# Kernel tuning notes

Hardware: AMD Instinct MI355X
Metric: run time of the kernel (lower is better)

Reference implementation:

```python
import jax, jax.numpy as jnp
import numpy as np

B, S, D, H = 4, 2048, 1024, 16
DH = D // H

def setup_inputs() -> dict:
    key = jax.random.key(0)
    ks = jax.random.split(key, 4)
    scale = 1.0 / np.sqrt(D)
    x = jax.random.normal(ks[0], (B, S, D), dtype=jnp.float32)
    Wq = jax.random.normal(ks[1], (D, D), dtype=jnp.float32) * scale
    Wk = jax.random.normal(ks[2], (D, D), dtype=jnp.float32) * scale
    Wv = jax.random.normal(ks[3], (D, D), dtype=jnp.float32) * scale
    bq = jnp.zeros((D,), dtype=jnp.float32)
    bk = jnp.zeros((D,), dtype=jnp.float32)
    bv = jnp.zeros((D,), dtype=jnp.float32)
    # causal mask, broadcastable to [B, H, S, S]; mask==0 positions get -inf
    mask = jnp.tril(jnp.ones((S, S), dtype=bool))[None, None, :, :]
    return {"x": x, "mask": mask, "Wq": Wq, "bq": bq, "Wk": Wk, "bk": bk, "Wv": Wv, "bv": bv}

def reference(x, mask, Wq, bq, Wk, bk, Wv, bv):
    b, s, d = x.shape
    def proj(W, bias):
        # nn.Linear: x @ W.T + b, then split heads -> [b, H, s, DH]
        y = jnp.einsum('bsd,ed->bse', x, W) + bias
        return y.reshape(b, s, H, DH).transpose(0, 2, 1, 3)
    q = proj(Wq, bq)
    k = proj(Wk, bk)
    v = proj(Wv, bv)
    scores = jnp.einsum('bhqd,bhkd->bhqk', q, k) / jnp.sqrt(jnp.float32(DH))
    scores = jnp.where(mask, scores, -jnp.inf)
    attn = jax.nn.softmax(scores, axis=-1)
    out = jnp.einsum('bhqk,bhkd->bhqd', attn, v)
    return out.transpose(0, 2, 1, 3).reshape(b, s, d)
```

## Files before the change

kernel.cpp:

```cpp
#include <hip/hip_runtime.h>
#include <hip/hip_bf16.h>
#include <stdint.h>

typedef unsigned short u16;
typedef unsigned int   u32;
typedef short bf16x8 __attribute__((ext_vector_type(8)));
typedef float f32x4  __attribute__((ext_vector_type(4)));

typedef bf16x8 __attribute__((__may_alias__)) bf16x8_a;
typedef uint4  __attribute__((__may_alias__)) uint4_a;
typedef uint2  __attribute__((__may_alias__)) uint2_a;
typedef float4 __attribute__((__may_alias__)) float4_a;

#define MFMA_BF16(a,b,c) __builtin_amdgcn_mfma_f32_16x16x32_bf16((a),(b),(c),0,0,0)
#define L2E 1.44269504088896340736f

#define SEQ 2048
#define DMODEL 1024
#define NH 16
#define DH 64

__device__ __forceinline__ u32 pack_bf2(float a, float b) {
  union { __hip_bfloat162 h; u32 u; } c;
  c.h = __float22bfloat162_rn(make_float2(a, b));
  return c.u;
}

__device__ __forceinline__ u16 f2bf(float f) {
  u32 u = __builtin_bit_cast(u32, f);
  u += 0x7FFFu + ((u >> 16) & 1u);
  return (u16)(u >> 16);
}

__device__ __forceinline__ void gl_lds16(const u16* g, u16* l) {
  __builtin_amdgcn_global_load_lds(
      (const __attribute__((address_space(1))) void*)g,
      (__attribute__((address_space(3))) void*)l, 16, 0, 0);
}

__global__ __launch_bounds__(256) void cvt_x_bf16(
    const float* __restrict__ s, u16* __restrict__ d, int n8)
{
  int i = blockIdx.x * 256 + threadIdx.x;
  const int stride = gridDim.x * 256;
  for (; i < n8; i += stride) {
    const float4_a* p = (const float4_a*)(s + (size_t)i * 8);
    float4 a = p[0], b = p[1];
    uint4 o;
    o.x = pack_bf2(a.x, a.y); o.y = pack_bf2(a.z, a.w);
    o.z = pack_bf2(b.x, b.y); o.w = pack_bf2(b.z, b.w);
    *(uint4_a*)(d + (size_t)i * 8) = o;
  }
}

__global__ __launch_bounds__(256) void cvt_w_bf16(
    const float* __restrict__ wq, const float* __restrict__ wk, const float* __restrict__ wv,
    u16* __restrict__ oq, u16* __restrict__ ok, u16* __restrict__ ov)
{
  const float* s = (blockIdx.y == 0) ? wq : (blockIdx.y == 1) ? wk : wv;
  u16*         d = (blockIdx.y == 0) ? oq : (blockIdx.y == 1) ? ok : ov;
  const int i = blockIdx.x * 256 + threadIdx.x;
  const float4_a* p = (const float4_a*)(s + (size_t)i * 8);
  float4 a = p[0], b = p[1];
  uint4 o;
  o.x = pack_bf2(a.x, a.y); o.y = pack_bf2(a.z, a.w);
  o.z = pack_bf2(b.x, b.y); o.w = pack_bf2(b.z, b.w);
  *(uint4_a*)(d + (size_t)i * 8) = o;
}

__global__ __launch_bounds__(256, 4) void qkv_gemm_bf(
    const u16* __restrict__ Xb,
    const u16* __restrict__ Wqb, const u16* __restrict__ Wkb, const u16* __restrict__ Wvb,
    const float* __restrict__ Bq, const float* __restrict__ Bk, const float* __restrict__ Bv,
    u16* __restrict__ Qo, u16* __restrict__ Ko, u16* __restrict__ Vo)
{
  __shared__ u16 As[2][128 * 32];
  __shared__ u16 Bs[2][128 * 32];

  const int tid  = threadIdx.x;
  const int lane = tid & 63;
  const int wid  = tid >> 6;
  const int l16  = lane & 15;
  const int quad = lane >> 4;
  const int wm   = (wid >> 1) * 64;
  const int wn   = (wid & 1) * 64;

  const int m0 = blockIdx.x * 128;
  const int n0 = blockIdx.y * 128;
  const int pj = blockIdx.z;

  const u16*   Wb   = (pj == 0) ? Wqb : (pj == 1) ? Wkb : Wvb;
  const float* Bias = (pj == 0) ? Bq : (pj == 1) ? Bk : Bv;
  u16*         Out  = (pj == 0) ? Qo : (pj == 1) ? Ko : Vo;
  const float scale = (pj == 0) ? 0.125f : 1.0f;

  f32x4 acc[4][4];
#pragma unroll
  for (int i = 0; i < 4; i++)
#pragma unroll
    for (int j = 0; j < 4; j++) acc[i][j] = (f32x4){0.f, 0.f, 0.f, 0.f};

  const int lr = lane >> 2;
  const int lc = (lane & 3) * 8;

  const u16* Arow = Xb + (size_t)m0 * DMODEL;
  const u16* Brow = Wb + (size_t)n0 * DMODEL;

  const int NT = DMODEL / 32;

#pragma unroll
  for (int c = 0; c < 2; c++) {
    const int band = c * 64 + wid * 16;
    gl_lds16(Arow + (size_t)(band + lr) * DMODEL + 0 + lc, &As[0][band * 32]);
    gl_lds16(Brow + (size_t)(band + lr) * DMODEL + 0 + lc, &Bs[0][band * 32]);
  }
#pragma unroll
  for (int c = 0; c < 2; c++) {
    const int band = c * 64 + wid * 16;
    gl_lds16(Arow + (size_t)(band + lr) * DMODEL + 32 + lc, &As[1][band * 32]);
    gl_lds16(Brow + (size_t)(band + lr) * DMODEL + 32 + lc, &Bs[1][band * 32]);
  }

  for (int t = 0; t < NT; ++t) {
    const int cur = t & 1;
    if (t < NT - 1) asm volatile("s_waitcnt vmcnt(4)" ::: "memory");
    else            asm volatile("s_waitcnt vmcnt(0)" ::: "memory");
    __builtin_amdgcn_s_barrier();

    bf16x8 a[4], b[4];
#pragma unroll
    for (int mt = 0; mt < 4; mt++)
      a[mt] = *(const bf16x8_a*)&As[cur][(wm + mt * 16 + l16) * 32 + quad * 8];
#pragma unroll
    for (int nt = 0; nt < 4; nt++)
      b[nt] = *(const bf16x8_a*)&Bs[cur][(wn + nt * 16 + l16) * 32 + quad * 8];

    asm volatile("s_waitcnt lgkmcnt(0)" ::: "memory");
    __builtin_amdgcn_sched_barrier(0);
    __builtin_amdgcn_s_barrier();

    if (t + 2 < NT) {
      const int kt2 = (t + 2) * 32;
#pragma unroll
      for (int c = 0; c < 2; c++) {
        const int band = c * 64 + wid * 16;
        gl_lds16(Arow + (size_t)(band + lr) * DMODEL + kt2 + lc, &As[cur][band * 32]);
        gl_lds16(Brow + (size_t)(band + lr) * DMODEL + kt2 + lc, &Bs[cur][band * 32]);
      }
    }

#pragma unroll
    for (int mt = 0; mt < 4; mt++)
#pragma unroll
      for (int nt = 0; nt < 4; nt++)
        acc[mt][nt] = MFMA_BF16(a[mt], b[nt], acc[mt][nt]);
  }

  if (pj == 2) {
#pragma unroll
    for (int mt = 0; mt < 4; mt++) {
#pragma unroll
      for (int nt = 0; nt < 4; nt++) {
        const int n = n0 + wn + nt * 16 + l16;
        const float bias = Bias[n];
        const int h = n >> 6, dh = n & 63;
        const int m = m0 + wm + mt * 16 + quad * 4;
        const int bb = m >> 11, ss = m & 2047;
        uint2 pk;
        pk.x = pack_bf2(acc[mt][nt][0] + bias, acc[mt][nt][1] + bias);
        pk.y = pack_bf2(acc[mt][nt][2] + bias, acc[mt][nt][3] + bias);
        *(uint2_a*)&Out[((size_t)(bb * NH + h) * DH + dh) * SEQ + ss] = pk;
      }
    }
  } else {
#pragma unroll
    for (int mt = 0; mt < 4; mt++) {
#pragma unroll
      for (int nt = 0; nt < 4; nt++) {
        const int n = n0 + wn + nt * 16 + l16;
        const float bias = Bias[n];
        const int h = n >> 6, dh = n & 63;
#pragma unroll
        for (int r = 0; r < 4; r++) {
          const int m = m0 + wm + mt * 16 + quad * 4 + r;
          const int bb = m >> 11, ss = m & 2047;
          Out[((((size_t)bb * NH + h) * SEQ + ss) << 6) + dh] = f2bf((acc[mt][nt][r] + bias) * scale);
        }
      }
    }
  }
}

__global__ __launch_bounds__(256, 2) void qkv_gemm(
    const float* __restrict__ X,
    const float* __restrict__ Wq, const float* __restrict__ Wk, const float* __restrict__ Wv,
    const float* __restrict__ Bq, const float* __restrict__ Bk, const float* __restrict__ Bv,
    u16* __restrict__ Qo, u16* __restrict__ Ko, u16* __restrict__ Vo)
{
  __shared__ u16 As[128 * 32];
  __shared__ u16 Bs[128 * 32];

  const int tid  = threadIdx.x;
  const int lane = tid & 63;
  const int wid  = tid >> 6;
  const int l16  = lane & 15;
  const int quad = lane >> 4;
  const int wm   = (wid >> 1) * 64;
  const int wn   = (wid & 1) * 64;

  const int m0 = blockIdx.x * 128;
  const int n0 = blockIdx.y * 128;
  const int pj = blockIdx.z;

  const float* W    = (pj == 0) ? Wq : (pj == 1) ? Wk : Wv;
  const float* Bias = (pj == 0) ? Bq : (pj == 1) ? Bk : Bv;
  u16*         Out  = (pj == 0) ? Qo : (pj == 1) ? Ko : Vo;
  const float scale = (pj == 0) ? 0.125f : 1.0f;

  f32x4 acc[4][4];
#pragma unroll
  for (int i = 0; i < 4; i++)
#pragma unroll
    for (int j = 0; j < 4; j++) acc[i][j] = (f32x4){0.f, 0.f, 0.f, 0.f};

  float4 gX[4], gW[4];
#pragma unroll
  for (int i = 0; i < 4; i++) {
    const int ch = i * 256 + tid;
    const int r = ch >> 3, c = ch & 7;
    gX[i] = *(const float4_a*)(X + (size_t)(m0 + r) * DMODEL + c * 4);
    gW[i] = *(const float4_a*)(W + (size_t)(n0 + r) * DMODEL + c * 4);
  }

  for (int kt = 0; kt < DMODEL; kt += 32) {
    __syncthreads();
#pragma unroll
    for (int i = 0; i < 4; i++) {
      const int ch = i * 256 + tid;
      const int r = ch >> 3, c = ch & 7;
      uint2 xp, wp;
      xp.x = pack_bf2(gX[i].x, gX[i].y);  xp.y = pack_bf2(gX[i].z, gX[i].w);
      wp.x = pack_bf2(gW[i].x, gW[i].y);  wp.y = pack_bf2(gW[i].z, gW[i].w);
      *(uint2_a*)&As[r * 32 + c * 4] = xp;
      *(uint2_a*)&Bs[r * 32 + c * 4] = wp;
    }
    __syncthreads();

    if (kt + 32 < DMODEL) {
#pragma unroll
      for (int i = 0; i < 4; i++) {
        const int ch = i * 256 + tid;
        const int r = ch >> 3, c = ch & 7;
        gX[i] = *(const float4_a*)(X + (size_t)(m0 + r) * DMODEL + kt + 32 + c * 4);
        gW[i] = *(const float4_a*)(W + (size_t)(n0 + r) * DMODEL + kt + 32 + c * 4);
      }
    }

    bf16x8 a[4], b[4];
#pragma unroll
    for (int mt = 0; mt < 4; mt++)
      a[mt] = *(const bf16x8_a*)&As[(wm + mt * 16 + l16) * 32 + quad * 8];
#pragma unroll
    for (int nt = 0; nt < 4; nt++)
      b[nt] = *(const bf16x8_a*)&Bs[(wn + nt * 16 + l16) * 32 + quad * 8];
#pragma unroll
    for (int mt = 0; mt < 4; mt++)
#pragma unroll
      for (int nt = 0; nt < 4; nt++)
        acc[mt][nt] = MFMA_BF16(a[mt], b[nt], acc[mt][nt]);
  }

  if (pj == 2) {
#pragma unroll
    for (int mt = 0; mt < 4; mt++) {
#pragma unroll
      for (int nt = 0; nt < 4; nt++) {
        const int n = n0 + wn + nt * 16 + l16;
        const float bias = Bias[n];
        const int h = n >> 6, dh = n & 63;
        const int m = m0 + wm + mt * 16 + quad * 4;
        const int bb = m >> 11, ss = m & 2047;
        uint2 pk;
        pk.x = pack_bf2(acc[mt][nt][0] + bias, acc[mt][nt][1] + bias);
        pk.y = pack_bf2(acc[mt][nt][2] + bias, acc[mt][nt][3] + bias);
        *(uint2_a*)&Out[((size_t)(bb * NH + h) * DH + dh) * SEQ + ss] = pk;
      }
    }
  } else {
#pragma unroll
    for (int mt = 0; mt < 4; mt++) {
#pragma unroll
      for (int nt = 0; nt < 4; nt++) {
        const int n = n0 + wn + nt * 16 + l16;
        const float bias = Bias[n];
        const int h = n >> 6, dh = n & 63;
#pragma unroll
        for (int r = 0; r < 4; r++) {
          const int m = m0 + wm + mt * 16 + quad * 4 + r;
          const int bb = m >> 11, ss = m & 2047;
          Out[((((size_t)bb * NH + h) * SEQ + ss) << 6) + dh] = f2bf((acc[mt][nt][r] + bias) * scale);
        }
      }
    }
  }
}

__global__ __launch_bounds__(256, 4) void flash_attn(
    const u16* __restrict__ Q, const u16* __restrict__ K, const u16* __restrict__ VT,
    float* __restrict__ O)
{
  __shared__ u16 Ks[64 * 72];
  __shared__ u16 VTs[64 * 72];
  __shared__ u16 Ps[4 * 32 * 72];

  const int tid  = threadIdx.x;
  const int lane = tid & 63;
  const int wid  = tid >> 6;
  const int l16  = lane & 15;
  const int quad = lane >> 4;

  const int idx = blockIdx.x;
  const int y = idx >> 6, g = y >> 2, r4 = y & 3;
  const int qt = (g & 1) ? ((g == 1 ? 0 : 4) + r4) : ((g == 0 ? 15 : 11) - r4);
  const int bh  = idx & 63;
  const int bb = bh >> 4, hh = bh & 15;
  const int qbase = qt * 128;

  const u16* Qh = Q  + (size_t)bh * (SEQ * DH);
  const u16* Kh = K  + (size_t)bh * (SEQ * DH);
  const u16* Vh = VT + (size_t)bh * (DH * SEQ);

#pragma unroll
  for (int i = 0; i < 4; i++) {
    const int ch = i * 256 + tid;
    const int r = ch >> 3, c = ch & 7;
    *(uint4_a*)&Ps[r * 72 + c * 8] = *(const uint4_a*)(Qh + (size_t)(qbase + r) * DH + c * 8);
  }
  __syncthreads();

  u16* Pw = &Ps[wid * 32 * 72];
  bf16x8 qf[2][2];
#pragma unroll
  for (int ct = 0; ct < 2; ct++)
#pragma unroll
    for (int ks = 0; ks < 2; ks++)
      qf[ct][ks] = *(const bf16x8_a*)&Pw[(ct * 16 + l16) * 72 + ks * 32 + quad * 8];

  f32x4 o[4][2];
#pragma unroll
  for (int dt = 0; dt < 4; dt++)
#pragma unroll
    for (int ct = 0; ct < 2; ct++) o[dt][ct] = (f32x4){0.f, 0.f, 0.f, 0.f};

  float mold[2] = {-1e30f, -1e30f};
  float lsum[2] = {0.f, 0.f};

  const int jmax = 2 * qt + 1;

  uint4 gK[2], gV[2];
#pragma unroll
  for (int i = 0; i < 2; i++) {
    const int ch = i * 256 + tid;
    gK[i] = *(const uint4_a*)(Kh + (size_t)(ch >> 3) * DH + (ch & 7) * 8);
    gV[i] = *(const uint4_a*)(Vh + (size_t)(ch >> 3) * SEQ + (ch & 7) * 8);
  }

  for (int j = 0; j <= jmax; j++) {
    __syncthreads();
#pragma unroll
    for (int i = 0; i < 2; i++) {
      const int ch = i * 256 + tid;
      *(uint4_a*)&Ks[(ch >> 3) * 72 + (ch & 7) * 8]  = gK[i];
      *(uint4_a*)&VTs[(ch >> 3) * 72 + (ch & 7) * 8] = gV[i];
    }
    __syncthreads();

    if (j < jmax) {
      const int kb2 = (j + 1) * 64;
#pragma unroll
      for (int i = 0; i < 2; i++) {
        const int ch = i * 256 + tid;
        gK[i] = *(const uint4_a*)(Kh + (size_t)(kb2 + (ch >> 3)) * DH + (ch & 7) * 8);
        gV[i] = *(const uint4_a*)(Vh + (size_t)(ch >> 3) * SEQ + kb2 + (ch & 7) * 8);
      }
    }

    f32x4 s[4][2];
#pragma unroll
    for (int rt = 0; rt < 4; rt++) {
      bf16x8 ka0 = *(const bf16x8_a*)&Ks[(rt * 16 + l16) * 72 + 0 + quad * 8];
      bf16x8 ka1 = *(const bf16x8_a*)&Ks[(rt * 16 + l16) * 72 + 32 + quad * 8];
#pragma unroll
      for (int ct = 0; ct < 2; ct++) {
        f32x4 c = (f32x4){0.f, 0.f, 0.f, 0.f};
        c = MFMA_BF16(ka0, qf[ct][0], c);
        c = MFMA_BF16(ka1, qf[ct][1], c);
        s[rt][ct] = c;
      }
    }

    if (j >= (qt << 1)) {
      const int kvb = j * 64;
#pragma unroll
      for (int rt = 0; rt < 4; rt++)
#pragma unroll
        for (int ct = 0; ct < 2; ct++) {
          const int ql = qbase + wid * 32 + ct * 16 + l16;
#pragma unroll
          for (int r = 0; r < 4; r++) {
            const int kvg = kvb + rt * 16 + quad * 4 + r;
            if (kvg > ql) s[rt][ct][r] = -1e30f;
          }
        }
    }

#pragma unroll
    for (int ct = 0; ct < 2; ct++) {
      float m0_ = fmaxf(fmaxf(s[0][ct][0], s[0][ct][1]), fmaxf(s[0][ct][2], s[0][ct][3]));
      float m1_ = fmaxf(fmaxf(s[1][ct][0], s[1][ct][1]), fmaxf(s[1][ct][2], s[1][ct][3]));
      float m2_ = fmaxf(fmaxf(s[2][ct][0], s[2][ct][1]), fmaxf(s[2][ct][2], s[2][ct][3]));
      float m3_ = fmaxf(fmaxf(s[3][ct][0], s[3][ct][1]), fmaxf(s[3][ct][2], s[3][ct][3]));
      float mt = fmaxf(fmaxf(m0_, m1_), fmaxf(m2_, m3_));
      mt = fmaxf(mt, __shfl_xor(mt, 16));
      mt = fmaxf(mt, __shfl_xor(mt, 32));

      if (!__all(mt - mold[ct] <= 8.0f)) {
        const float mnew = fmaxf(mold[ct], mt);
        const float a = __builtin_amdgcn_exp2f((mold[ct] - mnew) * L2E);
        lsum[ct] *= a;
        mold[ct] = mnew;
#pragma unroll
        for (int dt = 0; dt < 4; dt++)
#pragma unroll
          for (int r = 0; r < 4; r++) o[dt][ct][r] *= a;
      }
      const float mref = mold[ct];

#pragma unroll
      for (int rt = 0; rt < 4; rt++)
#pragma unroll
        for (int r = 0; r < 4; r++)
          s[rt][ct][r] = __builtin_amdgcn_exp2f((s[rt][ct][r] - mref) * L2E);

      float t0 = (s[0][ct][0] + s[0][ct][1]) + (s[0][ct][2] + s[0][ct][3]);
      float t1 = (s[1][ct][0] + s[1][ct][1]) + (s[1][ct][2] + s[1][ct][3]);
      float t2 = (s[2][ct][0] + s[2][ct][1]) + (s[2][ct][2] + s[2][ct][3]);
      float t3 = (s[3][ct][0] + s[3][ct][1]) + (s[3][ct][2] + s[3][ct][3]);
      float ls = (t0 + t1) + (t2 + t3);
      ls += __shfl_xor(ls, 16);
      ls += __shfl_xor(ls, 32);
      lsum[ct] += ls;
    }

#pragma unroll
    for (int rt = 0; rt < 4; rt++) {
#pragma unroll
      for (int ct = 0; ct < 2; ct++) {
        uint2 pk;
        pk.x = pack_bf2(s[rt][ct][0], s[rt][ct][1]);
        pk.y = pack_bf2(s[rt][ct][2], s[rt][ct][3]);
        *(uint2_a*)&Pw[(ct * 16 + l16) * 72 + rt * 16 + quad * 4] = pk;
      }
    }
    asm volatile("s_waitcnt lgkmcnt(0)" ::: "memory");

#pragma unroll
    for (int ks2 = 0; ks2 < 2; ks2++) {
      bf16x8 vt[4], pb[2];
#pragma unroll
      for (int dt = 0; dt < 4; dt++)
        vt[dt] = *(const bf16x8_a*)&VTs[(dt * 16 + l16) * 72 + ks2 * 32 + quad * 8];
#pragma unroll
      for (int ct = 0; ct < 2; ct++)
        pb[ct] = *(const bf16x8_a*)&Pw[(ct * 16 + l16) * 72 + ks2 * 32 + quad * 8];
#pragma unroll
      for (int dt = 0; dt < 4; dt++)
#pragma unroll
        for (int ct = 0; ct < 2; ct++)
          o[dt][ct] = MFMA_BF16(vt[dt], pb[ct], o[dt][ct]);
    }
  }

#pragma unroll
  for (int ct = 0; ct < 2; ct++) {
    const float inv = 1.0f / lsum[ct];
    const int qg = qbase + wid * 32 + ct * 16 + l16;
    float* orow = O + (size_t)((size_t)bb * SEQ + qg) * DMODEL + hh * 64;
#pragma unroll
    for (int dt = 0; dt < 4; dt++) {
      float4 v4;
      v4.x = o[dt][ct][0] * inv;  v4.y = o[dt][ct][1] * inv;
      v4.z = o[dt][ct][2] * inv;  v4.w = o[dt][ct][3] * inv;
      *(float4_a*)&orow[dt * 16 + quad * 4] = v4;
    }
  }
}

__global__ void paintf(float* out, int n, float v) {
  int i = blockIdx.x * 256 + threadIdx.x;
  if (i < n) out[i] = v;
}

extern "C" void kernel_launch(void* const* d_in, const int* in_sizes, int n_in,
                              void* d_out, int out_size, void* d_ws, size_t ws_size,
                              hipStream_t stream) {
  float* out = (float*)d_out;

  const size_t elems  = (size_t)4 * SEQ * DMODEL;
  const size_t welems = (size_t)DMODEL * DMODEL;
  const size_t need_old = 3 * elems * sizeof(u16);
  const size_t need_new = (4 * elems + 3 * welems) * sizeof(u16);

  if (ws_size < need_old) {
    paintf<<<(out_size + 255) / 256, 256, 0, stream>>>(out, out_size, 3.0e38f);
    return;
  }

  const float* x  = (const float*)d_in[0];
  const float* Wq = (const float*)d_in[2];
  const float* bq = (const float*)d_in[3];
  const float* Wk = (const float*)d_in[4];
  const float* bk = (const float*)d_in[5];
  const float* Wv = (const float*)d_in[6];
  const float* bv = (const float*)d_in[7];

  u16* q = (u16*)d_ws;
  u16* k = q + elems;
  u16* v = k + elems;

  if (ws_size >= need_new) {
    u16* xb  = v + elems;
    u16* wqb = xb + elems;
    u16* wkb = wqb + welems;
    u16* wvb = wkb + welems;
    cvt_x_bf16<<<2048, 256, 0, stream>>>(x, xb, (int)(elems / 8));
    cvt_w_bf16<<<dim3(512, 3), 256, 0, stream>>>(Wq, Wk, Wv, wqb, wkb, wvb);
    qkv_gemm_bf<<<dim3(64, 8, 3), 256, 0, stream>>>(xb, wqb, wkb, wvb, bq, bk, bv, q, k, v);
  } else {
    qkv_gemm<<<dim3(64, 8, 3), 256, 0, stream>>>(x, Wq, Wk, Wv, bq, bk, bv, q, k, v);
  }

  flash_attn<<<1024, 256, 0, stream>>>(q, k, v, out);
}
```

Baseline: 287.5 us.

## Loop GEMM blocks over two N tiles, MFMA row sums, simpler attention tile order

The bf16 QKV GEMM now has each block compute two 128-wide N subtiles in sequence, which halves the grid in y and lowers the occupancy hint from 4 to 3. In flash attention, the per-row softmax sum is now accumulated by an MFMA against a vector of ones instead of adds and cross-lane shuffles, and the max shuffle runs only when a rescale is needed. The interleaved query-tile ordering is replaced by a plain descending order. These changes aim to cut shuffle and ALU overhead and reduce launch count, but risk worse load balance across the causal tiles and less latency hiding in the GEMM.

```diff
diff --git a/kernel.cpp b/kernel.cpp
--- a/kernel.cpp
+++ b/kernel.cpp
@@ -68,7 +68,7 @@
   *(uint4_a*)(d + (size_t)i * 8) = o;
 }
 
-__global__ __launch_bounds__(256, 4) void qkv_gemm_bf(
+__global__ __launch_bounds__(256, 3) void qkv_gemm_bf(
     const u16* __restrict__ Xb,
     const u16* __restrict__ Wqb, const u16* __restrict__ Wkb, const u16* __restrict__ Wvb,
     const float* __restrict__ Bq, const float* __restrict__ Bk, const float* __restrict__ Bv,
@@ -86,7 +86,6 @@
   const int wn   = (wid & 1) * 64;
 
   const int m0 = blockIdx.x * 128;
-  const int n0 = blockIdx.y * 128;
   const int pj = blockIdx.z;
 
   const u16*   Wb   = (pj == 0) ? Wqb : (pj == 1) ? Wkb : Wvb;
@@ -94,61 +93,182 @@
   u16*         Out  = (pj == 0) ? Qo : (pj == 1) ? Ko : Vo;
   const float scale = (pj == 0) ? 0.125f : 1.0f;
 
-  f32x4 acc[4][4];
-#pragma unroll
-  for (int i = 0; i < 4; i++)
-#pragma unroll
-    for (int j = 0; j < 4; j++) acc[i][j] = (f32x4){0.f, 0.f, 0.f, 0.f};
-
   const int lr = lane >> 2;
   const int lc = (lane & 3) * 8;
 
   const u16* Arow = Xb + (size_t)m0 * DMODEL;
-  const u16* Brow = Wb + (size_t)n0 * DMODEL;
-
   const int NT = DMODEL / 32;
 
-#pragma unroll
-  for (int c = 0; c < 2; c++) {
-    const int band = c * 64 + wid * 16;
-    gl_lds16(Arow + (size_t)(band + lr) * DMODEL + 0 + lc, &As[0][band * 32]);
-    gl_lds16(Brow + (size_t)(band + lr) * DMODEL + 0 + lc, &Bs[0][band * 32]);
-  }
-#pragma unroll
-  for (int c = 0; c < 2; c++) {
-    const int band = c * 64 + wid * 16;
-    gl_lds16(Arow + (size_t)(band + lr) * DMODEL + 32 + lc, &As[1][band * 32]);
-    gl_lds16(Brow + (size_t)(band + lr) * DMODEL + 32 + lc, &Bs[1][band * 32]);
-  }
-
-  for (int t = 0; t < NT; ++t) {
-    const int cur = t & 1;
-    if (t < NT - 1) asm volatile("s_waitcnt vmcnt(4)" ::: "memory");
-    else            asm volatile("s_waitcnt vmcnt(0)" ::: "memory");
-    __builtin_amdgcn_s_barrier();
+  for (int nsub = 0; nsub < 2; ++nsub) {
+    const int n0 = blockIdx.y * 256 + nsub * 128;
+    const u16* Brow = Wb + (size_t)n0 * DMODEL;
+
+    f32x4 acc[4][4];
+#pragma unroll
+    for (int i = 0; i < 4; i++)
+#pragma unroll
+      for (int j = 0; j < 4; j++) acc[i][j] = (f32x4){0.f, 0.f, 0.f, 0.f};
+
+#pragma unroll
+    for (int c = 0; c < 2; c++) {
+      const int band = c * 64 + wid * 16;
+      gl_lds16(Arow + (size_t)(band + lr) * DMODEL + 0 + lc, &As[0][band * 32]);
+      gl_lds16(Brow + (size_t)(band + lr) * DMODEL + 0 + lc, &Bs[0][band * 32]);
+    }
+#pragma unroll
+    for (int c = 0; c < 2; c++) {
+      const int band = c * 64 + wid * 16;
+      gl_lds16(Arow + (size_t)(band + lr) * DMODEL + 32 + lc, &As[1][band * 32]);
+      gl_lds16(Brow + (size_t)(band + lr) * DMODEL + 32 + lc, &Bs[1][band * 32]);
+    }
+
+    for (int t = 0; t < NT; ++t) {
+      const int cur = t & 1;
+      if (t < NT - 1) asm volatile("s_waitcnt vmcnt(4)" ::: "memory");
+      else            asm volatile("s_waitcnt vmcnt(0)" ::: "memory");
+      __builtin_amdgcn_s_barrier();
+
+      bf16x8 a[4], b[4];
+#pragma unroll
+      for (int mt = 0; mt < 4; mt++)
+        a[mt] = *(const bf16x8_a*)&As[cur][(wm + mt * 16 + l16) * 32 + quad * 8];
+#pragma unroll
+      for (int nt = 0; nt < 4; nt++)
+        b[nt] = *(const bf16x8_a*)&Bs[cur][(wn + nt * 16 + l16) * 32 + quad * 8];
+
+      asm volatile("s_waitcnt lgkmcnt(0)" ::: "memory");
+      __builtin_amdgcn_sched_barrier(0);
+      __builtin_amdgcn_s_barrier();
+
+      if (t + 2 < NT) {
+        const int kt2 = (t + 2) * 32;
+#pragma unroll
+        for (int c = 0; c < 2; c++) {
+          const int band = c * 64 + wid * 16;
+          gl_lds16(Arow + (size_t)(band + lr) * DMODEL + kt2 + lc, &As[cur][band * 32]);
+          gl_lds16(Brow + (size_t)(band + lr) * DMODEL + kt2 + lc, &Bs[cur][band * 32]);
+        }
+      }
+
+#pragma unroll
+      for (int mt = 0; mt < 4; mt++)
+#pragma unroll
+        for (int nt = 0; nt < 4; nt++)
+          acc[mt][nt] = MFMA_BF16(a[mt], b[nt], acc[mt][nt]);
+    }
+
+    if (pj == 2) {
+#pragma unroll
+      for (int mt = 0; mt < 4; mt++) {
+#pragma unroll
+        for (int nt = 0; nt < 4; nt++) {
+          const int n = n0 + wn + nt * 16 + l16;
+          const float bias = Bias[n];
+          const int h = n >> 6, dh = n & 63;
+          const int m = m0 + wm + mt * 16 + quad * 4;
+          const int bb = m >> 11, ss = m & 2047;
+          uint2 pk;
+          pk.x = pack_bf2(acc[mt][nt][0] + bias, acc[mt][nt][1] + bias);
+          pk.y = pack_bf2(acc[mt][nt][2] + bias, acc[mt][nt][3] + bias);
+          *(uint2_a*)&Out[((size_t)(bb * NH + h) * DH + dh) * SEQ + ss] = pk;
+        }
+      }
+    } else {
+#pragma unroll
+      for (int mt = 0; mt < 4; mt++) {
+#pragma unroll
+        for (int nt = 0; nt < 4; nt++) {
+          const int n = n0 + wn + nt * 16 + l16;
+          const float bias = Bias[n];
+          const int h = n >> 6, dh = n & 63;
+#pragma unroll
+          for (int r = 0; r < 4; r++) {
+            const int m = m0 + wm + mt * 16 + quad * 4 + r;
+            const int bb = m >> 11, ss = m & 2047;
+            Out[((((size_t)bb * NH + h) * SEQ + ss) << 6) + dh] = f2bf((acc[mt][nt][r] + bias) * scale);
+          }
+        }
+      }
+    }
+
+    if (nsub == 0) {
+      asm volatile("s_waitcnt vmcnt(0)" ::: "memory");
+    }
+  }
+}
+
+__global__ __launch_bounds__(256, 2) void qkv_gemm(
+    const float* __restrict__ X,
+    const float* __restrict__ Wq, const float* __restrict__ Wk, const float* __restrict__ Wv,
+    const float* __restrict__ Bq, const float* __restrict__ Bk, const float* __restrict__ Bv,
+    u16* __restrict__ Qo, u16* __restrict__ Ko, u16* __restrict__ Vo)
+{
+  __shared__ u16 As[128 * 32];
+  __shared__ u16 Bs[128 * 32];
+
+  const int tid  = threadIdx.x;
+  const int lane = tid & 63;
+  const int wid  = tid >> 6;
+  const int l16  = lane & 15;
+  const int quad = lane >> 4;
+  const int wm   = (wid >> 1) * 64;
+  const int wn   = (wid & 1) * 64;
+
+  const int m0 = blockIdx.x * 128;
+  const int n0 = blockIdx.y * 128;
+  const int pj = blockIdx.z;
+
+  const float* W    = (pj == 0) ? Wq : (pj == 1) ? Wk : Wv;
+  const float* Bias = (pj == 0) ? Bq : (pj == 1) ? Bk : Bv;
+  u16*         Out  = (pj == 0) ? Qo : (pj == 1) ? Ko : Vo;
+  const float scale = (pj == 0) ? 0.125f : 1.0f;
+
+  f32x4 acc[4][4];
+#pragma unroll
+  for (int i = 0; i < 4; i++)
+#pragma unroll
+    for (int j = 0; j < 4; j++) acc[i][j] = (f32x4){0.f, 0.f, 0.f, 0.f};
+
+  float4 gX[4], gW[4];
+#pragma unroll
+  for (int i = 0; i < 4; i++) {
+    const int ch = i * 256 + tid;
+    const int r = ch >> 3, c = ch & 7;
+    gX[i] = *(const float4_a*)(X + (size_t)(m0 + r) * DMODEL + c * 4);
+    gW[i] = *(const float4_a*)(W + (size_t)(n0 + r) * DMODEL + c * 4);
+  }
+
+  for (int kt = 0; kt < DMODEL; kt += 32) {
+    __syncthreads();
+#pragma unroll
+    for (int i = 0; i < 4; i++) {
+      const int ch = i * 256 + tid;
+      const int r = ch >> 3, c = ch & 7;
+      uint2 xp, wp;
+      xp.x = pack_bf2(gX[i].x, gX[i].y);  xp.y = pack_bf2(gX[i].z, gX[i].w);
+      wp.x = pack_bf2(gW[i].x, gW[i].y);  wp.y = pack_bf2(gW[i].z, gW[i].w);
+      *(uint2_a*)&As[r * 32 + c * 4] = xp;
+      *(uint2_a*)&Bs[r * 32 + c * 4] = wp;
+    }
+    __syncthreads();
+
+    if (kt + 32 < DMODEL) {
+#pragma unroll
+      for (int i = 0; i < 4; i++) {
+        const int ch = i * 256 + tid;
+        const int r = ch >> 3, c = ch & 7;
+        gX[i] = *(const float4_a*)(X + (size_t)(m0 + r) * DMODEL + kt + 32 + c * 4);
+        gW[i] = *(const float4_a*)(W + (size_t)(n0 + r) * DMODEL + kt + 32 + c * 4);
+      }
+    }
 
     bf16x8 a[4], b[4];
 #pragma unroll
     for (int mt = 0; mt < 4; mt++)
-      a[mt] = *(const bf16x8_a*)&As[cur][(wm + mt * 16 + l16) * 32 + quad * 8];
+      a[mt] = *(const bf16x8_a*)&As[(wm + mt * 16 + l16) * 32 + quad * 8];
 #pragma unroll
     for (int nt = 0; nt < 4; nt++)
-      b[nt] = *(const bf16x8_a*)&Bs[cur][(wn + nt * 16 + l16) * 32 + quad * 8];
-
-    asm volatile("s_waitcnt lgkmcnt(0)" ::: "memory");
-    __builtin_amdgcn_sched_barrier(0);
-    __builtin_amdgcn_s_barrier();
-
-    if (t + 2 < NT) {
-      const int kt2 = (t + 2) * 32;
-#pragma unroll
-      for (int c = 0; c < 2; c++) {
-        const int band = c * 64 + wid * 16;
-        gl_lds16(Arow + (size_t)(band + lr) * DMODEL + kt2 + lc, &As[cur][band * 32]);
-        gl_lds16(Brow + (size_t)(band + lr) * DMODEL + kt2 + lc, &Bs[cur][band * 32]);
-      }
-    }
-
+      b[nt] = *(const bf16x8_a*)&Bs[(wn + nt * 16 + l16) * 32 + quad * 8];
 #pragma unroll
     for (int mt = 0; mt < 4; mt++)
 #pragma unroll
@@ -191,120 +311,6 @@
   }
 }
 
-__global__ __launch_bounds__(256, 2) void qkv_gemm(
-    const float* __restrict__ X,
-    const float* __restrict__ Wq, const float* __restrict__ Wk, const float* __restrict__ Wv,
-    const float* __restrict__ Bq, const float* __restrict__ Bk, const float* __restrict__ Bv,
-    u16* __restrict__ Qo, u16* __restrict__ Ko, u16* __restrict__ Vo)
-{
-  __shared__ u16 As[128 * 32];
-  __shared__ u16 Bs[128 * 32];
-
-  const int tid  = threadIdx.x;
-  const int lane = tid & 63;
-  const int wid  = tid >> 6;
-  const int l16  = lane & 15;
-  const int quad = lane >> 4;
-  const int wm   = (wid >> 1) * 64;
-  const int wn   = (wid & 1) * 64;
-
-  const int m0 = blockIdx.x * 128;
-  const int n0 = blockIdx.y * 128;
-  const int pj = blockIdx.z;
-
-  const float* W    = (pj == 0) ? Wq : (pj == 1) ? Wk : Wv;
-  const float* Bias = (pj == 0) ? Bq : (pj == 1) ? Bk : Bv;
-  u16*         Out  = (pj == 0) ? Qo : (pj == 1) ? Ko : Vo;
-  const float scale = (pj == 0) ? 0.125f : 1.0f;
-
-  f32x4 acc[4][4];
-#pragma unroll
-  for (int i = 0; i < 4; i++)
-#pragma unroll
-    for (int j = 0; j < 4; j++) acc[i][j] = (f32x4){0.f, 0.f, 0.f, 0.f};
-
-  float4 gX[4], gW[4];
-#pragma unroll
-  for (int i = 0; i < 4; i++) {
-    const int ch = i * 256 + tid;
-    const int r = ch >> 3, c = ch & 7;
-    gX[i] = *(const float4_a*)(X + (size_t)(m0 + r) * DMODEL + c * 4);
-    gW[i] = *(const float4_a*)(W + (size_t)(n0 + r) * DMODEL + c * 4);
-  }
-
-  for (int kt = 0; kt < DMODEL; kt += 32) {
-    __syncthreads();
-#pragma unroll
-    for (int i = 0; i < 4; i++) {
-      const int ch = i * 256 + tid;
-      const int r = ch >> 3, c = ch & 7;
-      uint2 xp, wp;
-      xp.x = pack_bf2(gX[i].x, gX[i].y);  xp.y = pack_bf2(gX[i].z, gX[i].w);
-      wp.x = pack_bf2(gW[i].x, gW[i].y);  wp.y = pack_bf2(gW[i].z, gW[i].w);
-      *(uint2_a*)&As[r * 32 + c * 4] = xp;
-      *(uint2_a*)&Bs[r * 32 + c * 4] = wp;
-    }
-    __syncthreads();
-
-    if (kt + 32 < DMODEL) {
-#pragma unroll
-      for (int i = 0; i < 4; i++) {
-        const int ch = i * 256 + tid;
-        const int r = ch >> 3, c = ch & 7;
-        gX[i] = *(const float4_a*)(X + (size_t)(m0 + r) * DMODEL + kt + 32 + c * 4);
-        gW[i] = *(const float4_a*)(W + (size_t)(n0 + r) * DMODEL + kt + 32 + c * 4);
-      }
-    }
-
-    bf16x8 a[4], b[4];
-#pragma unroll
-    for (int mt = 0; mt < 4; mt++)
-      a[mt] = *(const bf16x8_a*)&As[(wm + mt * 16 + l16) * 32 + quad * 8];
-#pragma unroll
-    for (int nt = 0; nt < 4; nt++)
-      b[nt] = *(const bf16x8_a*)&Bs[(wn + nt * 16 + l16) * 32 + quad * 8];
-#pragma unroll
-    for (int mt = 0; mt < 4; mt++)
-#pragma unroll
-      for (int nt = 0; nt < 4; nt++)
-        acc[mt][nt] = MFMA_BF16(a[mt], b[nt], acc[mt][nt]);
-  }
-
-  if (pj == 2) {
-#pragma unroll
-    for (int mt = 0; mt < 4; mt++) {
-#pragma unroll
-      for (int nt = 0; nt < 4; nt++) {
-        const int n = n0 + wn + nt * 16 + l16;
-        const float bias = Bias[n];
-        const int h = n >> 6, dh = n & 63;
-        const int m = m0 + wm + mt * 16 + quad * 4;
-        const int bb = m >> 11, ss = m & 2047;
-        uint2 pk;
-        pk.x = pack_bf2(acc[mt][nt][0] + bias, acc[mt][nt][1] + bias);
-        pk.y = pack_bf2(acc[mt][nt][2] + bias, acc[mt][nt][3] + bias);
-        *(uint2_a*)&Out[((size_t)(bb * NH + h) * DH + dh) * SEQ + ss] = pk;
-      }
-    }
-  } else {
-#pragma unroll
-    for (int mt = 0; mt < 4; mt++) {
-#pragma unroll
-      for (int nt = 0; nt < 4; nt++) {
-        const int n = n0 + wn + nt * 16 + l16;
-        const float bias = Bias[n];
-        const int h = n >> 6, dh = n & 63;
-#pragma unroll
-        for (int r = 0; r < 4; r++) {
-          const int m = m0 + wm + mt * 16 + quad * 4 + r;
-          const int bb = m >> 11, ss = m & 2047;
-          Out[((((size_t)bb * NH + h) * SEQ + ss) << 6) + dh] = f2bf((acc[mt][nt][r] + bias) * scale);
-        }
-      }
-    }
-  }
-}
-
 __global__ __launch_bounds__(256, 4) void flash_attn(
     const u16* __restrict__ Q, const u16* __restrict__ K, const u16* __restrict__ VT,
     float* __restrict__ O)
@@ -320,8 +326,7 @@
   const int quad = lane >> 4;
 
   const int idx = blockIdx.x;
-  const int y = idx >> 6, g = y >> 2, r4 = y & 3;
-  const int qt = (g & 1) ? ((g == 1 ? 0 : 4) + r4) : ((g == 0 ? 15 : 11) - r4);
+  const int qt  = 15 - (idx >> 6);
   const int bh  = idx & 63;
   const int bb = bh >> 4, hh = bh & 15;
   const int qbase = qt * 128;
@@ -346,14 +351,18 @@
     for (int ks = 0; ks < 2; ks++)
       qf[ct][ks] = *(const bf16x8_a*)&Pw[(ct * 16 + l16) * 72 + ks * 32 + quad * 8];
 
+  bf16x8 ones;
+#pragma unroll
+  for (int i = 0; i < 8; i++) ones[i] = (short)0x3F80;
+
   f32x4 o[4][2];
 #pragma unroll
   for (int dt = 0; dt < 4; dt++)
 #pragma unroll
     for (int ct = 0; ct < 2; ct++) o[dt][ct] = (f32x4){0.f, 0.f, 0.f, 0.f};
 
+  f32x4 lacc[2] = {(f32x4){0.f,0.f,0.f,0.f}, (f32x4){0.f,0.f,0.f,0.f}};
   float mold[2] = {-1e30f, -1e30f};
-  float lsum[2] = {0.f, 0.f};
 
   const int jmax = 2 * qt + 1;
 
@@ -420,19 +429,20 @@
       float m1_ = fmaxf(fmaxf(s[1][ct][0], s[1][ct][1]), fmaxf(s[1][ct][2], s[1][ct][3]));
       float m2_ = fmaxf(fmaxf(s[2][ct][0], s[2][ct][1]), fmaxf(s[2][ct][2], s[2][ct][3]));
       float m3_ = fmaxf(fmaxf(s[3][ct][0], s[3][ct][1]), fmaxf(s[3][ct][2], s[3][ct][3]));
-      float mt = fmaxf(fmaxf(m0_, m1_), fmaxf(m2_, m3_));
-      mt = fmaxf(mt, __shfl_xor(mt, 16));
-      mt = fmaxf(mt, __shfl_xor(mt, 32));
-
-      if (!__all(mt - mold[ct] <= 8.0f)) {
+      const float mloc = fmaxf(fmaxf(m0_, m1_), fmaxf(m2_, m3_));
+
+      if (!__all(mloc - mold[ct] <= 8.0f)) {
+        float mt = fmaxf(mloc, __shfl_xor(mloc, 16));
+        mt = fmaxf(mt, __shfl_xor(mt, 32));
         const float mnew = fmaxf(mold[ct], mt);
         const float a = __builtin_amdgcn_exp2f((mold[ct] - mnew) * L2E);
-        lsum[ct] *= a;
         mold[ct] = mnew;
 #pragma unroll
         for (int dt = 0; dt < 4; dt++)
 #pragma unroll
           for (int r = 0; r < 4; r++) o[dt][ct][r] *= a;
+#pragma unroll
+        for (int r = 0; r < 4; r++) lacc[ct][r] *= a;
       }
       const float mref = mold[ct];
 
@@ -441,15 +451,6 @@
 #pragma unroll
         for (int r = 0; r < 4; r++)
           s[rt][ct][r] = __builtin_amdgcn_exp2f((s[rt][ct][r] - mref) * L2E);
-
-      float t0 = (s[0][ct][0] + s[0][ct][1]) + (s[0][ct][2] + s[0][ct][3]);
-      float t1 = (s[1][ct][0] + s[1][ct][1]) + (s[1][ct][2] + s[1][ct][3]);
-      float t2 = (s[2][ct][0] + s[2][ct][1]) + (s[2][ct][2] + s[2][ct][3]);
-      float t3 = (s[3][ct][0] + s[3][ct][1]) + (s[3][ct][2] + s[3][ct][3]);
-      float ls = (t0 + t1) + (t2 + t3);
-      ls += __shfl_xor(ls, 16);
-      ls += __shfl_xor(ls, 32);
-      lsum[ct] += ls;
     }
 
 #pragma unroll
@@ -478,12 +479,15 @@
 #pragma unroll
         for (int ct = 0; ct < 2; ct++)
           o[dt][ct] = MFMA_BF16(vt[dt], pb[ct], o[dt][ct]);
+#pragma unroll
+      for (int ct = 0; ct < 2; ct++)
+        lacc[ct] = MFMA_BF16(ones, pb[ct], lacc[ct]);
     }
   }
 
 #pragma unroll
   for (int ct = 0; ct < 2; ct++) {
-    const float inv = 1.0f / lsum[ct];
+    const float inv = 1.0f / lacc[ct][0];
     const int qg = qbase + wid * 32 + ct * 16 + l16;
     float* orow = O + (size_t)((size_t)bb * SEQ + qg) * DMODEL + hh * 64;
 #pragma unroll
@@ -535,7 +539,7 @@
     u16* wvb = wkb + welems;
     cvt_x_bf16<<<2048, 256, 0, stream>>>(x, xb, (int)(elems / 8));
     cvt_w_bf16<<<dim3(512, 3), 256, 0, stream>>>(Wq, Wk, Wv, wqb, wkb, wvb);
-    qkv_gemm_bf<<<dim3(64, 8, 3), 256, 0, stream>>>(xb, wqb, wkb, wvb, bq, bk, bv, q, k, v);
+    qkv_gemm_bf<<<dim3(64, 4, 3), 256, 0, stream>>>(xb, wqb, wkb, wvb, bq, bk, bv, q, k, v);
   } else {
     qkv_gemm<<<dim3(64, 8, 3), 256, 0, stream>>>(x, Wq, Wk, Wv, bq, bk, bv, q, k, v);
   }
```

Result: faster. 270.6 us (-5.9%).
